# Performance work log

Measured on AMD Instinct MI355X. Metric: run time of the kernel, lower is better.

The kernel has to match this reference:

```python
import jax, jax.numpy as jnp
import numpy as np

B, S, D, H, HD, L, E, K, M, V = 1, 2048, 1024, 16, 64, 2, 8, 2, 768, 32000
EPS = 1e-06
THETA = 1000000.0


def rmsnorm(x, w, eps=EPS):
    xf = x.astype(jnp.float32)
    var = jnp.mean(xf * xf, axis=-1, keepdims=True)
    return (w * (xf * jax.lax.rsqrt(var + eps))).astype(x.dtype)


def apply_rope(x, cos, sin):
    # x: [B,S,H,HD], cos/sin: [S,HD]; rotate_half convention (HF Qwen3)
    c = cos[None, :, None, :]
    s = sin[None, :, None, :]
    x1, x2 = jnp.split(x, 2, axis=-1)
    rot = jnp.concatenate([-x2, x1], axis=-1)
    return x * c + rot * s


def setup_inputs() -> dict:
    key = jax.random.key(0)
    ks = jax.random.split(key, 16)
    std = 0.02
    inp = {}
    inp['input_ids'] = jax.random.randint(ks[0], (B, S), 0, V)
    inp['embed'] = jax.random.normal(ks[1], (V, D), jnp.float32) * std
    inp['wq'] = jax.random.normal(ks[2], (L, D, H * HD), jnp.float32) * std
    inp['wk'] = jax.random.normal(ks[3], (L, D, H * HD), jnp.float32) * std
    inp['wv'] = jax.random.normal(ks[4], (L, D, H * HD), jnp.float32) * std
    inp['wo'] = jax.random.normal(ks[5], (L, H * HD, D), jnp.float32) * std
    inp['q_norm_w'] = jnp.ones((L, HD), jnp.float32)
    inp['k_norm_w'] = jnp.ones((L, HD), jnp.float32)
    inp['attn_norm_w'] = jnp.ones((L, D), jnp.float32)
    inp['ffn_norm_w'] = jnp.ones((L, D), jnp.float32)
    inp['gate_w'] = jax.random.normal(ks[6], (L, D, E), jnp.float32) * std
    inp['w_gate'] = jax.random.normal(ks[7], (L, E, D, M), jnp.float32) * std
    inp['w_up'] = jax.random.normal(ks[8], (L, E, D, M), jnp.float32) * std
    inp['w_down'] = jax.random.normal(ks[9], (L, E, M, D), jnp.float32) * std
    inp['final_norm_w'] = jnp.ones((D,), jnp.float32)
    inp['out_w'] = jax.random.normal(ks[10], (D, V), jnp.float32) * (D ** -0.5)
    # rope cache: cos/sin with duplicated freqs (HF default rope)
    inv_freq = 1.0 / (THETA ** (jnp.arange(0, HD, 2, dtype=jnp.float32) / HD))
    freqs = jnp.outer(jnp.arange(S, dtype=jnp.float32), inv_freq)  # [S,HD/2]
    emb = jnp.concatenate([freqs, freqs], axis=-1)  # [S,HD]
    inp['cos'] = jnp.cos(emb)
    inp['sin'] = jnp.sin(emb)
    return inp


def reference(input_ids, embed, wq, wk, wv, wo, q_norm_w, k_norm_w, attn_norm_w,
              ffn_norm_w, gate_w, w_gate, w_up, w_down, final_norm_w, out_w, cos, sin):
    h = embed[input_ids]  # [B,S,D]
    causal = jnp.tril(jnp.ones((S, S), bool))[None, None]  # [1,1,S,S]
    scale = 1.0 / np.sqrt(HD)

    def layer(h, p):
        Wq, Wk, Wv, Wo, qn, kn, an, fn, gw, Wg, Wu, Wd = p
        # --- attention ---
        x = rmsnorm(h, an)
        q = (x @ Wq).reshape(B, S, H, HD)
        k = (x @ Wk).reshape(B, S, H, HD)
        v = (x @ Wv).reshape(B, S, H, HD)
        q = apply_rope(rmsnorm(q, qn), cos, sin)
        k = apply_rope(rmsnorm(k, kn), cos, sin)
        scores = jnp.einsum('bqhd,bkhd->bhqk', q, k) * scale
        scores = jnp.where(causal, scores, jnp.finfo(scores.dtype).min)
        attn = jax.nn.softmax(scores, axis=-1)
        o = jnp.einsum('bhqk,bkhd->bqhd', attn, v).reshape(B, S, H * HD) @ Wo
        h = h + o
        # --- sparse MoE ---
        x = rmsnorm(h, fn).reshape(-1, D)  # [T,D]
        probs = jax.nn.softmax((x @ gw).astype(jnp.float32), axis=-1)  # [T,E]
        vals, idx = jax.lax.top_k(probs, K)
        vals = vals / jnp.sum(vals, axis=-1, keepdims=True)  # norm_topk_prob=True
        T = x.shape[0]
        dense = jnp.zeros((T, E), x.dtype).at[jnp.arange(T)[:, None], idx].set(vals.astype(x.dtype))
        g = jnp.einsum('td,edm->tem', x, Wg)
        u = jnp.einsum('td,edm->tem', x, Wu)
        y = jnp.einsum('tem,emd->ted', jax.nn.silu(g) * u, Wd)
        moe = jnp.einsum('te,ted->td', dense, y).reshape(B, S, D)
        return h + moe, None

    h, _ = jax.lax.scan(layer, h, (wq, wk, wv, wo, q_norm_w, k_norm_w, attn_norm_w,
                                   ffn_norm_w, gate_w, w_gate, w_up, w_down))
    h = rmsnorm(h, final_norm_w)
    return h @ out_w  # [B,S,V]
```

## Files before the change

### kernel.cpp

```cpp
#include <hip/hip_runtime.h>
#include <hip/hip_bf16.h>


constexpr int S_ = 2048, D_ = 1024, H_ = 16, HD_ = 64, E_ = 8, MF_ = 768, V_ = 32000;

typedef short  short8 __attribute__((ext_vector_type(8)));
typedef float  f32x4  __attribute__((ext_vector_type(4)));

static __device__ __forceinline__ unsigned short f2bf(float f) {
    unsigned u = __float_as_uint(f);
    u += 0x7FFF + ((u >> 16) & 1);
    return (unsigned short)(u >> 16);
}

static __device__ __forceinline__ short8 u2s8(uint4 u) {
    union { uint4 a; short8 b; } x; x.a = u; return x.b;
}

__global__ __launch_bounds__(256) void k_gather(const int* __restrict__ ids,
                                                const float* __restrict__ emb,
                                                float* __restrict__ h) {
    int tok = blockIdx.x;
    int id  = ids[tok];
    const float4* src = (const float4*)(emb + (long)id * D_);
    float4*       dst = (float4*)(h + (long)tok * D_);
    dst[threadIdx.x] = src[threadIdx.x];
}

template <int BF>
__global__ __launch_bounds__(256) void k_rmsnorm(const float* __restrict__ in,
                                                 const float* __restrict__ w,
                                                 float* __restrict__ outf,
                                                 unsigned short* __restrict__ outb) {
    int row = blockIdx.x, t = threadIdx.x;
    float4 x = ((const float4*)(in + (long)row * D_))[t];
    float ss = x.x * x.x + x.y * x.y + x.z * x.z + x.w * x.w;
#pragma unroll
    for (int m = 32; m >= 1; m >>= 1) ss += __shfl_xor(ss, m);
    __shared__ float ps[4];
    if ((t & 63) == 0) ps[t >> 6] = ss;
    __syncthreads();
    float tot   = ps[0] + ps[1] + ps[2] + ps[3];
    float scale = 1.0f / sqrtf(tot * (1.0f / D_) + 1e-6f);
    float4 wv = ((const float4*)w)[t];
    float4 o;
    o.x = x.x * scale * wv.x; o.y = x.y * scale * wv.y;
    o.z = x.z * scale * wv.z; o.w = x.w * scale * wv.w;
    if (BF) {
        ushort4 ub;
        ub.x = f2bf(o.x); ub.y = f2bf(o.y); ub.z = f2bf(o.z); ub.w = f2bf(o.w);
        *(ushort4*)(outb + (long)row * D_ + t * 4) = ub;
    } else {
        ((float4*)(outf + (long)row * D_))[t] = o;
    }
}

__global__ __launch_bounds__(256) void k_qkrope(float* __restrict__ q, float* __restrict__ k,
                                                const float* __restrict__ qn,
                                                const float* __restrict__ kn,
                                                const float* __restrict__ cosb,
                                                const float* __restrict__ sinb) {
    int wid  = (blockIdx.x << 2) | (threadIdx.x >> 6);
    int lane = threadIdx.x & 63;
    int tensor = wid >> 15;
    int rem    = wid & 32767;
    int tok = rem >> 4, head = rem & 15;
    float* ptr = tensor ? k : q;
    const float* nw = tensor ? kn : qn;
    long off = ((long)tok * H_ + head) * HD_ + lane;
    float v = ptr[off];
    float ss = v * v;
#pragma unroll
    for (int m = 32; m >= 1; m >>= 1) ss += __shfl_xor(ss, m);
    float xn = v * (1.0f / sqrtf(ss * (1.0f / HD_) + 1e-6f)) * nw[lane];
    float other = __shfl_xor(xn, 32);
    float rot = (lane < 32) ? -other : other;
    ptr[off] = xn * cosb[tok * HD_ + lane] + rot * sinb[tok * HD_ + lane];
}

static __device__ __forceinline__ void splitpack2(float x0, float x1,
                                                  unsigned& wh, unsigned& wm,
                                                  unsigned& wl) {
    unsigned u0 = __float_as_uint(x0), u1 = __float_as_uint(x1);
    unsigned h0 = u0 & 0xFFFF0000u,    h1 = u1 & 0xFFFF0000u;
    float r0 = x0 - __uint_as_float(h0), r1 = x1 - __uint_as_float(h1);
    unsigned m0 = __float_as_uint(r0) & 0xFFFF0000u;
    unsigned m1 = __float_as_uint(r1) & 0xFFFF0000u;
    float s0 = r0 - __uint_as_float(m0), s1 = r1 - __uint_as_float(m1);
    unsigned l0 = __float_as_uint(s0),   l1 = __float_as_uint(s1);
    wh = (h0 >> 16) | h1;
    wm = (m0 >> 16) | m1;
    wl = (l0 >> 16) | (l1 & 0xFFFF0000u);
}

static __device__ __forceinline__ void split8(const float* v,
                                              uint4& qh, uint4& qm, uint4& ql) {
    unsigned ph[4], pm[4], pl[4];
#pragma unroll
    for (int j = 0; j < 4; j++) splitpack2(v[2 * j], v[2 * j + 1], ph[j], pm[j], pl[j]);
    qh = make_uint4(ph[0], ph[1], ph[2], ph[3]);
    qm = make_uint4(pm[0], pm[1], pm[2], pm[3]);
    ql = make_uint4(pl[0], pl[1], pl[2], pl[3]);
}

template <int IND, int EPI>
__global__ __launch_bounds__(256) void k_gemm_s6(const float* __restrict__ A,
                                                 const float* __restrict__ B0,
                                                 const float* __restrict__ B1,
                                                 const float* __restrict__ B2,
                                                 float* __restrict__ C,
                                                 const int* __restrict__ offs,
                                                 const int* __restrict__ rows,
                                                 const float* __restrict__ rwgt,
                                                 float* __restrict__ hout,
                                                 int Mtot, int N, int K,
                                                 long bStrideZ, long cStrideZ) {
    int z = blockIdx.z;
    int ms, me;
    if (offs) { ms = offs[z]; me = offs[z + 1]; }
    else      { ms = 0; me = Mtot; }
    int p0 = ms + blockIdx.y * 128;
    if (p0 >= me) return;
    const float* Bz;
    if (B1) Bz = (z == 0) ? B0 : (z == 1) ? B1 : B2;
    else    Bz = B0 + (long)z * bStrideZ;
    float* Cz = C ? (C + (long)z * cStrideZ) : nullptr;
    int n0 = blockIdx.x * 128;

    __shared__ __align__(16) unsigned short As[3][128][40];
    __shared__ __align__(16) unsigned short Bs[3][128][40];

    int t = threadIdx.x;
    int lane = t & 63, wave = t >> 6;
    int wm = (wave >> 1) * 64, wn = (wave & 1) * 64;
    int ln = lane & 15, lq = lane >> 4;

    f32x4 acc[4][4];
    f32x4 zero4 = {0.f, 0.f, 0.f, 0.f};
#pragma unroll
    for (int r = 0; r < 4; r++)
#pragma unroll
        for (int c = 0; c < 4; c++) acc[r][c] = zero4;

    int arow = t >> 1, ak0 = (t & 1) * 16;
    const float* aptr = nullptr;
    {
        int pA = p0 + arow;
        if (pA < me) {
            int srow = IND ? rows[pA] : pA;
            aptr = A + (long)srow * K + ak0;
        }
    }
    int brow = t >> 1, bk0 = (t & 1) * 16;
    const float* bbase = Bz + (n0 + brow);

    for (int k0 = 0; k0 < K; k0 += 32) {
        float va[16];
        if (aptr) {
#pragma unroll
            for (int c4 = 0; c4 < 4; c4++) {
                float4 f = *(const float4*)(aptr + k0 + c4 * 4);
                va[c4 * 4 + 0] = f.x; va[c4 * 4 + 1] = f.y;
                va[c4 * 4 + 2] = f.z; va[c4 * 4 + 3] = f.w;
            }
        } else {
#pragma unroll
            for (int j = 0; j < 16; j++) va[j] = 0.f;
        }
        uint4 ah0, am0, al0, ah1, am1, al1;
        split8(va,     ah0, am0, al0);
        split8(va + 8, ah1, am1, al1);
        float vb[16];
        {
            const float* bp = bbase + (long)(k0 + bk0) * N;
#pragma unroll
            for (int j = 0; j < 16; j++) vb[j] = bp[(long)j * N];
        }
        uint4 bh0, bm0, bl0, bh1, bm1, bl1;
        split8(vb,     bh0, bm0, bl0);
        split8(vb + 8, bh1, bm1, bl1);

        __syncthreads();
        *(uint4*)&As[0][arow][ak0]     = ah0;
        *(uint4*)&As[0][arow][ak0 + 8] = ah1;
        *(uint4*)&As[1][arow][ak0]     = am0;
        *(uint4*)&As[1][arow][ak0 + 8] = am1;
        *(uint4*)&As[2][arow][ak0]     = al0;
        *(uint4*)&As[2][arow][ak0 + 8] = al1;
        *(uint4*)&Bs[0][brow][bk0]     = bh0;
        *(uint4*)&Bs[0][brow][bk0 + 8] = bh1;
        *(uint4*)&Bs[1][brow][bk0]     = bm0;
        *(uint4*)&Bs[1][brow][bk0 + 8] = bm1;
        *(uint4*)&Bs[2][brow][bk0]     = bl0;
        *(uint4*)&Bs[2][brow][bk0 + 8] = bl1;
        __syncthreads();

        short8 fah[4], fam[4], fal[4];
#pragma unroll
        for (int r = 0; r < 4; r++) {
            fah[r] = *(const short8*)&As[0][wm + 16 * r + ln][lq * 8];
            fam[r] = *(const short8*)&As[1][wm + 16 * r + ln][lq * 8];
            fal[r] = *(const short8*)&As[2][wm + 16 * r + ln][lq * 8];
        }
#pragma unroll
        for (int c = 0; c < 4; c++) {
            short8 fbh = *(const short8*)&Bs[0][wn + 16 * c + ln][lq * 8];
            short8 fbm = *(const short8*)&Bs[1][wn + 16 * c + ln][lq * 8];
            short8 fbl = *(const short8*)&Bs[2][wn + 16 * c + ln][lq * 8];
#pragma unroll
            for (int r = 0; r < 4; r++) {
                f32x4 a2 = acc[r][c];
                a2 = __builtin_amdgcn_mfma_f32_16x16x32_bf16(fah[r], fbh, a2, 0, 0, 0);
                a2 = __builtin_amdgcn_mfma_f32_16x16x32_bf16(fah[r], fbm, a2, 0, 0, 0);
                a2 = __builtin_amdgcn_mfma_f32_16x16x32_bf16(fam[r], fbh, a2, 0, 0, 0);
                a2 = __builtin_amdgcn_mfma_f32_16x16x32_bf16(fah[r], fbl, a2, 0, 0, 0);
                a2 = __builtin_amdgcn_mfma_f32_16x16x32_bf16(fam[r], fbm, a2, 0, 0, 0);
                a2 = __builtin_amdgcn_mfma_f32_16x16x32_bf16(fal[r], fbh, a2, 0, 0, 0);
                acc[r][c] = a2;
            }
        }
    }

#pragma unroll
    for (int r = 0; r < 4; r++)
#pragma unroll
        for (int c = 0; c < 4; c++) {
            int rowb = wm + 16 * r + lq * 4;
            int col  = n0 + wn + 16 * c + ln;
#pragma unroll
            for (int i = 0; i < 4; i++) {
                int p = p0 + rowb + i;
                if (p >= me) continue;
                if (EPI == 2) {
                    atomicAdd(hout + (long)rows[p] * N + col, rwgt[p] * acc[r][c][i]);
                } else if (EPI == 1) {
                    float* cp = Cz + (long)p * N + col;
                    *cp += acc[r][c][i];
                } else {
                    Cz[(long)p * N + col] = acc[r][c][i];
                }
            }
        }
}

__global__ __launch_bounds__(256) void k_attn_mfma(const float* __restrict__ q,
                                                   const float* __restrict__ k,
                                                   const float* __restrict__ v,
                                                   float* __restrict__ o) {
    int head = blockIdx.y;
    int qi = ((blockIdx.y >> 3) & 1) ? (int)(gridDim.x - 1 - blockIdx.x) : (int)blockIdx.x;
    int q0 = qi * 64;

    __shared__ __align__(16) unsigned short Ks[3][64][72];
    __shared__ __align__(16) unsigned short Vt[3][64][72];
    __shared__ __align__(16) float Ps[64][68];

    int t = threadIdx.x;
    int lane = t & 63, w = t >> 6;
    int ln = lane & 15, lq = lane >> 4;

    short8 qh[2], qm[2], qlr[2];
    {
        const float* qp = q + ((long)(q0 + 16 * w + ln) * H_ + head) * HD_;
#pragma unroll
        for (int ks = 0; ks < 2; ks++) {
            float vq[8];
            float4 f0 = *(const float4*)(qp + 32 * ks + lq * 8);
            float4 f1 = *(const float4*)(qp + 32 * ks + lq * 8 + 4);
            vq[0] = f0.x; vq[1] = f0.y; vq[2] = f0.z; vq[3] = f0.w;
            vq[4] = f1.x; vq[5] = f1.y; vq[6] = f1.z; vq[7] = f1.w;
            uint4 hh, mm, ll;
            split8(vq, hh, mm, ll);
            qh[ks] = u2s8(hh); qm[ks] = u2s8(mm); qlr[ks] = u2s8(ll);
        }
    }

    f32x4 oc[4];
    f32x4 zero4 = {0.f, 0.f, 0.f, 0.f};
#pragma unroll
    for (int c = 0; c < 4; c++) oc[c] = zero4;
    float m_run[4], l_run[4];
#pragma unroll
    for (int i = 0; i < 4; i++) { m_run[i] = -3.402823466e38f; l_run[i] = 0.f; }

    for (int kt = 0; kt <= qi; kt++) {
        __syncthreads();
        {
            int kr = t >> 2, kq4 = (t & 3) * 16;
            const float* kp = k + ((long)(kt * 64 + kr) * H_ + head) * HD_ + kq4;
            float vk[16];
#pragma unroll
            for (int j = 0; j < 4; j++) {
                float4 f = *(const float4*)(kp + 4 * j);
                vk[4 * j + 0] = f.x; vk[4 * j + 1] = f.y;
                vk[4 * j + 2] = f.z; vk[4 * j + 3] = f.w;
            }
            uint4 h0, m0, l0, h1, m1, l1;
            split8(vk,     h0, m0, l0);
            split8(vk + 8, h1, m1, l1);
            *(uint4*)&Ks[0][kr][kq4]     = h0; *(uint4*)&Ks[0][kr][kq4 + 8] = h1;
            *(uint4*)&Ks[1][kr][kq4]     = m0; *(uint4*)&Ks[1][kr][kq4 + 8] = m1;
            *(uint4*)&Ks[2][kr][kq4]     = l0; *(uint4*)&Ks[2][kr][kq4 + 8] = l1;
            const float* vp = v + ((long)(kt * 64 + lane) * H_ + head) * HD_ + w * 16;
            float vvv[16];
#pragma unroll
            for (int j = 0; j < 4; j++) {
                float4 f = *(const float4*)(vp + 4 * j);
                vvv[4 * j + 0] = f.x; vvv[4 * j + 1] = f.y;
                vvv[4 * j + 2] = f.z; vvv[4 * j + 3] = f.w;
            }
#pragma unroll
            for (int j = 0; j < 16; j++) {
                float x = vvv[j];
                unsigned uu = __float_as_uint(x);
                unsigned hh = uu & 0xFFFF0000u;
                float rr = x - __uint_as_float(hh);
                unsigned mm2 = __float_as_uint(rr) & 0xFFFF0000u;
                float ss2 = rr - __uint_as_float(mm2);
                Vt[0][w * 16 + j][lane] = (unsigned short)(hh >> 16);
                Vt[1][w * 16 + j][lane] = (unsigned short)(mm2 >> 16);
                Vt[2][w * 16 + j][lane] = (unsigned short)(__float_as_uint(ss2) >> 16);
            }
        }
        __syncthreads();

        f32x4 sc[4];
#pragma unroll
        for (int c = 0; c < 4; c++) sc[c] = zero4;
#pragma unroll
        for (int ks = 0; ks < 2; ks++) {
#pragma unroll
            for (int c = 0; c < 4; c++) {
                const int co = 16 * c + ln, ko = 32 * ks + lq * 8;
                short8 bh = *(const short8*)&Ks[0][co][ko];
                short8 bm = *(const short8*)&Ks[1][co][ko];
                short8 bl = *(const short8*)&Ks[2][co][ko];
                f32x4 a2 = sc[c];
                a2 = __builtin_amdgcn_mfma_f32_16x16x32_bf16(qh[ks],  bh, a2, 0, 0, 0);
                a2 = __builtin_amdgcn_mfma_f32_16x16x32_bf16(qh[ks],  bm, a2, 0, 0, 0);
                a2 = __builtin_amdgcn_mfma_f32_16x16x32_bf16(qm[ks],  bh, a2, 0, 0, 0);
                a2 = __builtin_amdgcn_mfma_f32_16x16x32_bf16(qh[ks],  bl, a2, 0, 0, 0);
                a2 = __builtin_amdgcn_mfma_f32_16x16x32_bf16(qm[ks],  bm, a2, 0, 0, 0);
                a2 = __builtin_amdgcn_mfma_f32_16x16x32_bf16(qlr[ks], bh, a2, 0, 0, 0);
                sc[c] = a2;
            }
        }

#pragma unroll
        for (int i = 0; i < 4; i++) {
            int qg = q0 + 16 * w + 4 * lq + i;
            float mx = -3.402823466e38f;
#pragma unroll
            for (int c = 0; c < 4; c++) {
                int kvg = kt * 64 + 16 * c + ln;
                float s = sc[c][i] * 0.125f;
                s = (kvg <= qg) ? s : -3.402823466e38f;
                sc[c][i] = s;
                mx = fmaxf(mx, s);
            }
            mx = fmaxf(mx, __shfl_xor(mx, 1));
            mx = fmaxf(mx, __shfl_xor(mx, 2));
            mx = fmaxf(mx, __shfl_xor(mx, 4));
            mx = fmaxf(mx, __shfl_xor(mx, 8));
            float mn = fmaxf(m_run[i], mx);
            float al = expf(m_run[i] - mn);
            m_run[i] = mn;
            float sum = 0.f;
#pragma unroll
            for (int c = 0; c < 4; c++) {
                float e = expf(sc[c][i] - mn);
                Ps[16 * w + 4 * lq + i][16 * c + ln] = e;
                sum += e;
            }
            sum += __shfl_xor(sum, 1);
            sum += __shfl_xor(sum, 2);
            sum += __shfl_xor(sum, 4);
            sum += __shfl_xor(sum, 8);
            l_run[i] = l_run[i] * al + sum;
#pragma unroll
            for (int c = 0; c < 4; c++) oc[c][i] *= al;
        }

#pragma unroll
        for (int ks = 0; ks < 2; ks++) {
            float pv8[8];
            *(float4*)&pv8[0] = *(const float4*)&Ps[16 * w + ln][32 * ks + lq * 8];
            *(float4*)&pv8[4] = *(const float4*)&Ps[16 * w + ln][32 * ks + lq * 8 + 4];
            uint4 ph4, pm4, pl4;
            split8(pv8, ph4, pm4, pl4);
            short8 pah = u2s8(ph4), pam = u2s8(pm4), pal = u2s8(pl4);
#pragma unroll
            for (int c = 0; c < 4; c++) {
                const int co = 16 * c + ln, ko = 32 * ks + lq * 8;
                short8 bh = *(const short8*)&Vt[0][co][ko];
                short8 bm = *(const short8*)&Vt[1][co][ko];
                short8 bl = *(const short8*)&Vt[2][co][ko];
                f32x4 a2 = oc[c];
                a2 = __builtin_amdgcn_mfma_f32_16x16x32_bf16(pah, bh, a2, 0, 0, 0);
                a2 = __builtin_amdgcn_mfma_f32_16x16x32_bf16(pah, bm, a2, 0, 0, 0);
                a2 = __builtin_amdgcn_mfma_f32_16x16x32_bf16(pam, bh, a2, 0, 0, 0);
                a2 = __builtin_amdgcn_mfma_f32_16x16x32_bf16(pah, bl, a2, 0, 0, 0);
                a2 = __builtin_amdgcn_mfma_f32_16x16x32_bf16(pam, bm, a2, 0, 0, 0);
                a2 = __builtin_amdgcn_mfma_f32_16x16x32_bf16(pal, bh, a2, 0, 0, 0);
                oc[c] = a2;
            }
        }
    }

#pragma unroll
    for (int i = 0; i < 4; i++) {
        float invl = 1.0f / l_run[i];
        int qg = q0 + 16 * w + 4 * lq + i;
        float* op = o + ((long)qg * H_ + head) * HD_;
#pragma unroll
        for (int c = 0; c < 4; c++) op[16 * c + ln] = oc[c][i] * invl;
    }
}

__global__ __launch_bounds__(256) void k_router(const float* __restrict__ x,
                                                const float* __restrict__ gw,
                                                int* __restrict__ idx, float* __restrict__ wgt,
                                                int* __restrict__ cnt) {
    int tok  = (blockIdx.x << 2) | (threadIdx.x >> 6);
    int lane = threadIdx.x & 63;
    float acc[8] = {0.f, 0.f, 0.f, 0.f, 0.f, 0.f, 0.f, 0.f};
    for (int i = 0; i < 16; i++) {
        int d = lane + i * 64;
        float xv = x[(long)tok * D_ + d];
        const float* gp = gw + (long)d * E_;
#pragma unroll
        for (int e = 0; e < 8; e++) acc[e] = fmaf(xv, gp[e], acc[e]);
    }
#pragma unroll
    for (int e = 0; e < 8; e++)
#pragma unroll
        for (int m = 32; m >= 1; m >>= 1) acc[e] += __shfl_xor(acc[e], m);
    if (lane == 0) {
        int i1 = 0; float m1 = acc[0];
        for (int e = 1; e < 8; e++) if (acc[e] > m1) { m1 = acc[e]; i1 = e; }
        int i2 = -1; float m2 = -3.402823466e38f;
        for (int e = 0; e < 8; e++) if (e != i1 && acc[e] > m2) { m2 = acc[e]; i2 = e; }
        float w1 = 1.0f / (1.0f + expf(m2 - m1));
        idx[tok * 2] = i1; idx[tok * 2 + 1] = i2;
        wgt[tok * 2] = w1; wgt[tok * 2 + 1] = 1.0f - w1;
        atomicAdd(&cnt[i1], 1);
        atomicAdd(&cnt[i2], 1);
    }
}

__global__ void k_offsets(const int* __restrict__ cnt, int* __restrict__ off) {
    if (threadIdx.x == 0) {
        int run = 0;
        for (int e = 0; e < 8; e++) { off[e] = run; run += cnt[e]; }
        off[8] = run;
    }
}

__global__ __launch_bounds__(256) void k_scatter(const int* __restrict__ idx,
                                                 const float* __restrict__ wgt,
                                                 const int* __restrict__ off,
                                                 int* __restrict__ fill,
                                                 int* __restrict__ rows,
                                                 float* __restrict__ rwgt) {
    int tok = blockIdx.x * 256 + threadIdx.x;
#pragma unroll
    for (int j = 0; j < 2; j++) {
        int e = idx[tok * 2 + j];
        int pos = off[e] + atomicAdd(&fill[e], 1);
        rows[pos] = tok;
        rwgt[pos] = wgt[tok * 2 + j];
    }
}

__global__ __launch_bounds__(256) void k_silumul(const float* __restrict__ g,
                                                 const float* __restrict__ u,
                                                 float* __restrict__ z) {
    long i = (long)(blockIdx.x * 256 + threadIdx.x) * 4;
    float4 gv = *(const float4*)(g + i);
    float4 uv = *(const float4*)(u + i);
    float4 zv;
    zv.x = gv.x / (1.f + expf(-gv.x)) * uv.x;
    zv.y = gv.y / (1.f + expf(-gv.y)) * uv.y;
    zv.z = gv.z / (1.f + expf(-gv.z)) * uv.z;
    zv.w = gv.w / (1.f + expf(-gv.w)) * uv.w;
    *(float4*)(z + i) = zv;
}

__global__ __launch_bounds__(256) void k_transcast(const float* __restrict__ in,
                                                   unsigned short* __restrict__ out) {
    int c0 = blockIdx.x * 32;
    int r0 = blockIdx.y * 32;
    __shared__ __align__(16) float T[32][36];
    int t = threadIdx.x;
    {
        int row = t >> 3, cq = (t & 7) * 4;
        *(float4*)&T[row][cq] = *(const float4*)(in + (long)(r0 + row) * V_ + c0 + cq);
    }
    __syncthreads();
    {
        int n = t >> 3, kq = (t & 7) * 4;
        ushort4 u;
        u.x = f2bf(T[kq + 0][n]); u.y = f2bf(T[kq + 1][n]);
        u.z = f2bf(T[kq + 2][n]); u.w = f2bf(T[kq + 3][n]);
        *(ushort4*)(out + (long)(c0 + n) * D_ + r0 + kq) = u;
    }
}

__global__ __launch_bounds__(256) void k_gemm_bf16(const unsigned short* __restrict__ A,
                                                   const unsigned short* __restrict__ BT,
                                                   float* __restrict__ C) {
    int m0 = blockIdx.x * 128, n0 = blockIdx.y * 128;
    __shared__ __align__(16) unsigned short As[128][40];
    __shared__ __align__(16) unsigned short Bs[128][40];
    int t = threadIdx.x;
    int lane = t & 63, wave = t >> 6;
    int wm = (wave >> 1) * 64, wn = (wave & 1) * 64;
    int ln = lane & 15, lq = lane >> 4;
    f32x4 acc[4][4];
    f32x4 zero4 = {0.f, 0.f, 0.f, 0.f};
#pragma unroll
    for (int r = 0; r < 4; r++)
#pragma unroll
        for (int c = 0; c < 4; c++) acc[r][c] = zero4;
    int rowA = t >> 1;
    int q1 = (t * 2) & 3, q2 = (t * 2 + 1) & 3;
    for (int k0 = 0; k0 < 1024; k0 += 32) {
        const uint4* ap = (const uint4*)(A + (long)(m0 + rowA) * 1024 + k0);
        const uint4* bp = (const uint4*)(BT + (long)(n0 + rowA) * 1024 + k0);
        uint4 a0 = ap[q1], a1 = ap[q2];
        uint4 b0 = bp[q1], b1 = bp[q2];
        __syncthreads();
        *(uint4*)&As[rowA][q1 * 8] = a0;
        *(uint4*)&As[rowA][q2 * 8] = a1;
        *(uint4*)&Bs[rowA][q1 * 8] = b0;
        *(uint4*)&Bs[rowA][q2 * 8] = b1;
        __syncthreads();
        short8 a[4], b[4];
#pragma unroll
        for (int r = 0; r < 4; r++) a[r] = *(const short8*)&As[wm + 16 * r + ln][lq * 8];
#pragma unroll
        for (int c = 0; c < 4; c++) b[c] = *(const short8*)&Bs[wn + 16 * c + ln][lq * 8];
#pragma unroll
        for (int r = 0; r < 4; r++)
#pragma unroll
            for (int c = 0; c < 4; c++)
                acc[r][c] = __builtin_amdgcn_mfma_f32_16x16x32_bf16(a[r], b[c], acc[r][c], 0, 0, 0);
    }
#pragma unroll
    for (int r = 0; r < 4; r++)
#pragma unroll
        for (int c = 0; c < 4; c++) {
            int row = m0 + wm + 16 * r + lq * 4;
            int col = n0 + wn + 16 * c + ln;
#pragma unroll
            for (int i = 0; i < 4; i++)
                C[(long)(row + i) * V_ + col] = acc[r][c][i];
        }
}

extern "C" void kernel_launch(void* const* d_in, const int* in_sizes, int n_in,
                              void* d_out, int out_size, void* d_ws, size_t ws_size,
                              hipStream_t stream) {
    (void)in_sizes; (void)n_in; (void)out_size; (void)ws_size;
    const int*   ids   = (const int*)d_in[0];
    const float* embed = (const float*)d_in[1];
    const float* wq    = (const float*)d_in[2];
    const float* wk    = (const float*)d_in[3];
    const float* wv    = (const float*)d_in[4];
    const float* wo    = (const float*)d_in[5];
    const float* qnw   = (const float*)d_in[6];
    const float* knw   = (const float*)d_in[7];
    const float* anw   = (const float*)d_in[8];
    const float* fnw   = (const float*)d_in[9];
    const float* gatew = (const float*)d_in[10];
    const float* wgate = (const float*)d_in[11];
    const float* wup   = (const float*)d_in[12];
    const float* wdown = (const float*)d_in[13];
    const float* finw  = (const float*)d_in[14];
    const float* outw  = (const float*)d_in[15];
    const float* cosb  = (const float*)d_in[16];
    const float* sinb  = (const float*)d_in[17];
    float* out = (float*)d_out;

    char* w = (char*)d_ws;
    float* h  = (float*)(w);
    float* x  = (float*)(w + 8388608);
    float* q  = (float*)(w + 16777216);
    float* kk = (float*)(w + 25165824);
    float* vv = (float*)(w + 33554432);
    float* ao = (float*)(w + 41943040);
    float* g  = (float*)(w + 50331648);
    float* u  = (float*)(w + 62914560);
    float* z  = (float*)(w + 75497472);
    unsigned short* hn  = (unsigned short*)(w + 88080384);
    unsigned short* owT = (unsigned short*)(w + 16777216);
    char* rbase = w + 92274688;
    int*   idx  = (int*)(rbase);
    float* wgt  = (float*)(rbase + 16384);
    int*   cnt  = (int*)(rbase + 32768);
    int*   fill = (int*)(rbase + 32768 + 32);
    int*   offs = (int*)(rbase + 32768 + 64);
    int*   rows = (int*)(rbase + 32768 + 128);
    float* rwgt = (float*)(rbase + 32768 + 128 + 16384);

    k_gather<<<2048, 256, 0, stream>>>(ids, embed, h);

    for (int l = 0; l < 2; l++) {
        const float* wq_l = wq + (long)l * D_ * D_;
        const float* wk_l = wk + (long)l * D_ * D_;
        const float* wv_l = wv + (long)l * D_ * D_;
        const float* wo_l = wo + (long)l * D_ * D_;
        const float* an_l = anw + l * D_;
        const float* fn_l = fnw + l * D_;
        const float* qn_l = qnw + l * HD_;
        const float* kn_l = knw + l * HD_;
        const float* gw_l = gatew + (long)l * D_ * E_;
        const float* wg_l = wgate + (long)l * E_ * D_ * MF_;
        const float* wu_l = wup   + (long)l * E_ * D_ * MF_;
        const float* wd_l = wdown + (long)l * E_ * MF_ * D_;

        k_rmsnorm<0><<<2048, 256, 0, stream>>>(h, an_l, x, nullptr);
        k_gemm_s6<0, 0><<<dim3(8, 16, 3), 256, 0, stream>>>(x, wq_l, wk_l, wv_l, q,
            nullptr, nullptr, nullptr, nullptr, 2048, 1024, 1024, 0, 2048L * 1024);
        k_qkrope<<<16384, 256, 0, stream>>>(q, kk, qn_l, kn_l, cosb, sinb);
        k_attn_mfma<<<dim3(32, 16), 256, 0, stream>>>(q, kk, vv, ao);
        k_gemm_s6<0, 1><<<dim3(8, 16, 1), 256, 0, stream>>>(ao, wo_l, nullptr, nullptr, h,
            nullptr, nullptr, nullptr, nullptr, 2048, 1024, 1024, 0, 0);
        k_rmsnorm<0><<<2048, 256, 0, stream>>>(h, fn_l, x, nullptr);
        hipMemsetAsync(cnt, 0, 64, stream);
        k_router<<<512, 256, 0, stream>>>(x, gw_l, idx, wgt, cnt);
        k_offsets<<<1, 64, 0, stream>>>(cnt, offs);
        k_scatter<<<8, 256, 0, stream>>>(idx, wgt, offs, fill, rows, rwgt);
        k_gemm_s6<1, 0><<<dim3(6, 16, 8), 256, 0, stream>>>(x, wg_l, nullptr, nullptr, g,
            offs, rows, nullptr, nullptr, 4096, 768, 1024, (long)D_ * MF_, 0);
        k_gemm_s6<1, 0><<<dim3(6, 16, 8), 256, 0, stream>>>(x, wu_l, nullptr, nullptr, u,
            offs, rows, nullptr, nullptr, 4096, 768, 1024, (long)D_ * MF_, 0);
        k_silumul<<<3072, 256, 0, stream>>>(g, u, z);
        k_gemm_s6<0, 2><<<dim3(8, 16, 8), 256, 0, stream>>>(z, wd_l, nullptr, nullptr, nullptr,
            offs, rows, rwgt, h, 4096, 1024, 768, (long)MF_ * D_, 0);
    }

    k_rmsnorm<1><<<2048, 256, 0, stream>>>(h, finw, nullptr, hn);
    k_transcast<<<dim3(1000, 32), 256, 0, stream>>>(outw, owT);
    k_gemm_bf16<<<dim3(16, 250), 256, 0, stream>>>(hn, owT, out);
}
```

Before: 2.131 ms.

## Load GEMM A fragments directly from global and double-buffer B tiles

The split-bf16 grouped GEMM now loads A rows straight from global memory into MFMA fragments and splits them in registers, which removes the A shared-memory tile. B tiles are double-buffered in LDS so the next tile loads while the current one computes, with one barrier per half-step. The bf16 logits GEMM drops LDS entirely and register-prefetches fragments from global, ping-ponging between two sets. The cost is redundant global loads across waves that share rows, since there is no LDS reuse, and higher register pressure.

```diff
diff --git a/kernel.cpp b/kernel.cpp
--- a/kernel.cpp
+++ b/kernel.cpp
@@ -127,8 +127,7 @@
     float* Cz = C ? (C + (long)z * cStrideZ) : nullptr;
     int n0 = blockIdx.x * 128;
 
-    __shared__ __align__(16) unsigned short As[3][128][40];
-    __shared__ __align__(16) unsigned short Bs[3][128][40];
+    __shared__ __align__(16) unsigned short Bs[2][3][128][40];
 
     int t = threadIdx.x;
     int lane = t & 63, wave = t >> 6;
@@ -142,71 +141,56 @@
 #pragma unroll
         for (int c = 0; c < 4; c++) acc[r][c] = zero4;
 
-    int arow = t >> 1, ak0 = (t & 1) * 16;
-    const float* aptr = nullptr;
-    {
-        int pA = p0 + arow;
-        if (pA < me) {
-            int srow = IND ? rows[pA] : pA;
-            aptr = A + (long)srow * K + ak0;
+    const float* aptr[4];
+#pragma unroll
+    for (int r = 0; r < 4; r++) {
+        int p = p0 + wm + 16 * r + ln;
+        aptr[r] = nullptr;
+        if (p < me) {
+            int srow = IND ? rows[p] : p;
+            aptr[r] = A + (long)srow * K + lq * 8;
         }
     }
     int brow = t >> 1, bk0 = (t & 1) * 16;
     const float* bbase = Bz + (n0 + brow);
 
-    for (int k0 = 0; k0 < K; k0 += 32) {
-        float va[16];
-        if (aptr) {
-#pragma unroll
-            for (int c4 = 0; c4 < 4; c4++) {
-                float4 f = *(const float4*)(aptr + k0 + c4 * 4);
-                va[c4 * 4 + 0] = f.x; va[c4 * 4 + 1] = f.y;
-                va[c4 * 4 + 2] = f.z; va[c4 * 4 + 3] = f.w;
-            }
-        } else {
-#pragma unroll
-            for (int j = 0; j < 16; j++) va[j] = 0.f;
-        }
-        uint4 ah0, am0, al0, ah1, am1, al1;
-        split8(va,     ah0, am0, al0);
-        split8(va + 8, ah1, am1, al1);
+    auto bload = [&](int kk, uint4* bh, uint4* bm, uint4* bl) {
         float vb[16];
-        {
-            const float* bp = bbase + (long)(k0 + bk0) * N;
-#pragma unroll
-            for (int j = 0; j < 16; j++) vb[j] = bp[(long)j * N];
-        }
-        uint4 bh0, bm0, bl0, bh1, bm1, bl1;
-        split8(vb,     bh0, bm0, bl0);
-        split8(vb + 8, bh1, bm1, bl1);
-
-        __syncthreads();
-        *(uint4*)&As[0][arow][ak0]     = ah0;
-        *(uint4*)&As[0][arow][ak0 + 8] = ah1;
-        *(uint4*)&As[1][arow][ak0]     = am0;
-        *(uint4*)&As[1][arow][ak0 + 8] = am1;
-        *(uint4*)&As[2][arow][ak0]     = al0;
-        *(uint4*)&As[2][arow][ak0 + 8] = al1;
-        *(uint4*)&Bs[0][brow][bk0]     = bh0;
-        *(uint4*)&Bs[0][brow][bk0 + 8] = bh1;
-        *(uint4*)&Bs[1][brow][bk0]     = bm0;
-        *(uint4*)&Bs[1][brow][bk0 + 8] = bm1;
-        *(uint4*)&Bs[2][brow][bk0]     = bl0;
-        *(uint4*)&Bs[2][brow][bk0 + 8] = bl1;
-        __syncthreads();
-
-        short8 fah[4], fam[4], fal[4];
+        const float* bp = bbase + (long)(kk + bk0) * N;
+#pragma unroll
+        for (int j = 0; j < 16; j++) vb[j] = bp[(long)j * N];
+        split8(vb,     bh[0], bm[0], bl[0]);
+        split8(vb + 8, bh[1], bm[1], bl[1]);
+    };
+    auto bwrite = [&](int buf, const uint4* bh, const uint4* bm, const uint4* bl) {
+        *(uint4*)&Bs[buf][0][brow][bk0]     = bh[0];
+        *(uint4*)&Bs[buf][0][brow][bk0 + 8] = bh[1];
+        *(uint4*)&Bs[buf][1][brow][bk0]     = bm[0];
+        *(uint4*)&Bs[buf][1][brow][bk0 + 8] = bm[1];
+        *(uint4*)&Bs[buf][2][brow][bk0]     = bl[0];
+        *(uint4*)&Bs[buf][2][brow][bk0 + 8] = bl[1];
+    };
+    auto aload = [&](int kk, short8* fah, short8* fam, short8* fal) {
 #pragma unroll
         for (int r = 0; r < 4; r++) {
-            fah[r] = *(const short8*)&As[0][wm + 16 * r + ln][lq * 8];
-            fam[r] = *(const short8*)&As[1][wm + 16 * r + ln][lq * 8];
-            fal[r] = *(const short8*)&As[2][wm + 16 * r + ln][lq * 8];
-        }
+            float va[8] = {0.f, 0.f, 0.f, 0.f, 0.f, 0.f, 0.f, 0.f};
+            if (aptr[r]) {
+                float4 f0 = *(const float4*)(aptr[r] + kk);
+                float4 f1 = *(const float4*)(aptr[r] + kk + 4);
+                va[0] = f0.x; va[1] = f0.y; va[2] = f0.z; va[3] = f0.w;
+                va[4] = f1.x; va[5] = f1.y; va[6] = f1.z; va[7] = f1.w;
+            }
+            uint4 hh, mm, ll;
+            split8(va, hh, mm, ll);
+            fah[r] = u2s8(hh); fam[r] = u2s8(mm); fal[r] = u2s8(ll);
+        }
+    };
+    auto domfma = [&](int buf, const short8* fah, const short8* fam, const short8* fal) {
 #pragma unroll
         for (int c = 0; c < 4; c++) {
-            short8 fbh = *(const short8*)&Bs[0][wn + 16 * c + ln][lq * 8];
-            short8 fbm = *(const short8*)&Bs[1][wn + 16 * c + ln][lq * 8];
-            short8 fbl = *(const short8*)&Bs[2][wn + 16 * c + ln][lq * 8];
+            short8 fbh = *(const short8*)&Bs[buf][0][wn + 16 * c + ln][lq * 8];
+            short8 fbm = *(const short8*)&Bs[buf][1][wn + 16 * c + ln][lq * 8];
+            short8 fbl = *(const short8*)&Bs[buf][2][wn + 16 * c + ln][lq * 8];
 #pragma unroll
             for (int r = 0; r < 4; r++) {
                 f32x4 a2 = acc[r][c];
@@ -219,6 +203,30 @@
                 acc[r][c] = a2;
             }
         }
+    };
+
+    {
+        uint4 bh[2], bm[2], bl[2];
+        bload(0, bh, bm, bl);
+        bwrite(0, bh, bm, bl);
+    }
+    __syncthreads();
+
+    for (int k0 = 0; k0 < K; k0 += 64) {
+        short8 fah[4], fam[4], fal[4];
+        uint4 bh[2], bm[2], bl[2];
+        aload(k0, fah, fam, fal);
+        bload(k0 + 32, bh, bm, bl);
+        domfma(0, fah, fam, fal);
+        bwrite(1, bh, bm, bl);
+        __syncthreads();
+        aload(k0 + 32, fah, fam, fal);
+        int kn = k0 + 64;
+        bool more = kn < K;
+        if (more) bload(kn, bh, bm, bl);
+        domfma(1, fah, fam, fal);
+        if (more) bwrite(0, bh, bm, bl);
+        __syncthreads();
     }
 
 #pragma unroll
@@ -510,8 +518,6 @@
                                                    const unsigned short* __restrict__ BT,
                                                    float* __restrict__ C) {
     int m0 = blockIdx.x * 128, n0 = blockIdx.y * 128;
-    __shared__ __align__(16) unsigned short As[128][40];
-    __shared__ __align__(16) unsigned short Bs[128][40];
     int t = threadIdx.x;
     int lane = t & 63, wave = t >> 6;
     int wm = (wave >> 1) * 64, wn = (wave & 1) * 64;
@@ -522,30 +528,44 @@
     for (int r = 0; r < 4; r++)
 #pragma unroll
         for (int c = 0; c < 4; c++) acc[r][c] = zero4;
-    int rowA = t >> 1;
-    int q1 = (t * 2) & 3, q2 = (t * 2 + 1) & 3;
-    for (int k0 = 0; k0 < 1024; k0 += 32) {
-        const uint4* ap = (const uint4*)(A + (long)(m0 + rowA) * 1024 + k0);
-        const uint4* bp = (const uint4*)(BT + (long)(n0 + rowA) * 1024 + k0);
-        uint4 a0 = ap[q1], a1 = ap[q2];
-        uint4 b0 = bp[q1], b1 = bp[q2];
-        __syncthreads();
-        *(uint4*)&As[rowA][q1 * 8] = a0;
-        *(uint4*)&As[rowA][q2 * 8] = a1;
-        *(uint4*)&Bs[rowA][q1 * 8] = b0;
-        *(uint4*)&Bs[rowA][q2 * 8] = b1;
-        __syncthreads();
-        short8 a[4], b[4];
-#pragma unroll
-        for (int r = 0; r < 4; r++) a[r] = *(const short8*)&As[wm + 16 * r + ln][lq * 8];
-#pragma unroll
-        for (int c = 0; c < 4; c++) b[c] = *(const short8*)&Bs[wn + 16 * c + ln][lq * 8];
+
+    const unsigned short* ap[4];
+    const unsigned short* bp[4];
+#pragma unroll
+    for (int r = 0; r < 4; r++) ap[r] = A  + (long)(m0 + wm + 16 * r + ln) * 1024 + lq * 8;
+#pragma unroll
+    for (int c = 0; c < 4; c++) bp[c] = BT + (long)(n0 + wn + 16 * c + ln) * 1024 + lq * 8;
+
+    short8 a0[4], b0[4], a1[4], b1[4];
+#pragma unroll
+    for (int r = 0; r < 4; r++) a0[r] = *(const short8*)(ap[r]);
+#pragma unroll
+    for (int c = 0; c < 4; c++) b0[c] = *(const short8*)(bp[c]);
+
+#pragma unroll 1
+    for (int k0 = 0; k0 < 1024; k0 += 64) {
+        int k1 = k0 + 32;
+#pragma unroll
+        for (int r = 0; r < 4; r++) a1[r] = *(const short8*)(ap[r] + k1);
+#pragma unroll
+        for (int c = 0; c < 4; c++) b1[c] = *(const short8*)(bp[c] + k1);
 #pragma unroll
         for (int r = 0; r < 4; r++)
 #pragma unroll
             for (int c = 0; c < 4; c++)
-                acc[r][c] = __builtin_amdgcn_mfma_f32_16x16x32_bf16(a[r], b[c], acc[r][c], 0, 0, 0);
-    }
+                acc[r][c] = __builtin_amdgcn_mfma_f32_16x16x32_bf16(a0[r], b0[c], acc[r][c], 0, 0, 0);
+        int k2 = (k0 + 64) & 1023;
+#pragma unroll
+        for (int r = 0; r < 4; r++) a0[r] = *(const short8*)(ap[r] + k2);
+#pragma unroll
+        for (int c = 0; c < 4; c++) b0[c] = *(const short8*)(bp[c] + k2);
+#pragma unroll
+        for (int r = 0; r < 4; r++)
+#pragma unroll
+            for (int c = 0; c < 4; c++)
+                acc[r][c] = __builtin_amdgcn_mfma_f32_16x16x32_bf16(a1[r], b1[c], acc[r][c], 0, 0, 0);
+    }
+
 #pragma unroll
     for (int r = 0; r < 4; r++)
 #pragma unroll
```

Result: slower. 3.336 ms (+56.6%).

## Pre-split and transpose weights into bf16 planes before each GEMM

Applied to the files above, without the earlier changes.

Adds a k_wsplit kernel that transposes each fp32 weight matrix and splits it into hi/mid/lo bf16 planes laid out N-major. The GEMM then loads B tiles with contiguous 16-byte vector loads instead of strided scalar fp32 loads followed by per-block splitting. This removes redundant splitting across M-tiles and uncoalesced B reads. The cost is extra launches and a full read and write of the weights every call, and plane buffers are aliased into workspace regions, which risks overlap.

```diff
diff --git a/kernel.cpp b/kernel.cpp
--- a/kernel.cpp
+++ b/kernel.cpp
@@ -103,27 +103,54 @@
     ql = make_uint4(pl[0], pl[1], pl[2], pl[3]);
 }
 
+__global__ __launch_bounds__(256) void k_wsplit(const float* __restrict__ in,
+                                                unsigned short* __restrict__ out,
+                                                int N, int K,
+                                                long inStrideZ, long outStrideZ) {
+    int z = blockIdx.z;
+    const float* inz = in + (long)z * inStrideZ;
+    unsigned short* outz = out + (long)z * outStrideZ;
+    int n0 = blockIdx.x * 32, k0 = blockIdx.y * 32;
+    __shared__ float T[32][33];
+    int t = threadIdx.x;
+    {
+        int row = t >> 3, c4 = (t & 7) * 4;
+        *(float4*)&T[row][c4] = *(const float4*)(inz + (long)(k0 + row) * N + n0 + c4);
+    }
+    __syncthreads();
+    int n = t >> 3, kq = (t & 7) * 4;
+    float v0 = T[kq][n], v1 = T[kq + 1][n], v2 = T[kq + 2][n], v3 = T[kq + 3][n];
+    unsigned h01, m01, l01, h23, m23, l23;
+    splitpack2(v0, v1, h01, m01, l01);
+    splitpack2(v2, v3, h23, m23, l23);
+    long base = (long)(n0 + n) * K + k0 + kq;
+    long pk = (long)N * K;
+    *(uint2*)(outz + base)          = make_uint2(h01, h23);
+    *(uint2*)(outz + pk + base)     = make_uint2(m01, m23);
+    *(uint2*)(outz + 2 * pk + base) = make_uint2(l01, l23);
+}
+
 template <int IND, int EPI>
 __global__ __launch_bounds__(256) void k_gemm_s6(const float* __restrict__ A,
-                                                 const float* __restrict__ B0,
-                                                 const float* __restrict__ B1,
-                                                 const float* __restrict__ B2,
+                                                 const unsigned short* __restrict__ BplA,
+                                                 const unsigned short* __restrict__ BplB,
+                                                 int zsplit,
                                                  float* __restrict__ C,
                                                  const int* __restrict__ offs,
                                                  const int* __restrict__ rows,
                                                  const float* __restrict__ rwgt,
                                                  float* __restrict__ hout,
                                                  int Mtot, int N, int K,
-                                                 long bStrideZ, long cStrideZ) {
+                                                 long cStrideZ) {
     int z = blockIdx.z;
     int ms, me;
     if (offs) { ms = offs[z]; me = offs[z + 1]; }
     else      { ms = 0; me = Mtot; }
     int p0 = ms + blockIdx.y * 128;
     if (p0 >= me) return;
-    const float* Bz;
-    if (B1) Bz = (z == 0) ? B0 : (z == 1) ? B1 : B2;
-    else    Bz = B0 + (long)z * bStrideZ;
+    long planeSz = (long)N * K;
+    const unsigned short* bpl = (z < zsplit) ? BplA + (long)z * 3 * planeSz
+                                             : BplB + (long)(z - zsplit) * 3 * planeSz;
     float* Cz = C ? (C + (long)z * cStrideZ) : nullptr;
     int n0 = blockIdx.x * 128;
 
@@ -142,17 +169,28 @@
 #pragma unroll
         for (int c = 0; c < 4; c++) acc[r][c] = zero4;
 
-    int arow = t >> 1, ak0 = (t & 1) * 16;
+    int arow = t >> 1, ak0 = (t & 1) * 8;
+    arow = t >> 1; int akf = (t & 1) * 16;
     const float* aptr = nullptr;
     {
         int pA = p0 + arow;
         if (pA < me) {
             int srow = IND ? rows[pA] : pA;
-            aptr = A + (long)srow * K + ak0;
-        }
-    }
-    int brow = t >> 1, bk0 = (t & 1) * 16;
-    const float* bbase = Bz + (n0 + brow);
+            aptr = A + (long)srow * K + akf;
+        }
+    }
+    (void)ak0;
+
+    const unsigned short* bsrc[6];
+    unsigned short* bdst[6];
+#pragma unroll
+    for (int j = 0; j < 6; j++) {
+        int id = t + 256 * j;
+        int plane = id >> 9, rem = id & 511;
+        int brow = rem >> 2, bq = rem & 3;
+        bsrc[j] = bpl + (long)plane * planeSz + (long)(n0 + brow) * K + bq * 8;
+        bdst[j] = &Bs[plane][brow][bq * 8];
+    }
 
     for (int k0 = 0; k0 < K; k0 += 32) {
         float va[16];
@@ -170,29 +208,19 @@
         uint4 ah0, am0, al0, ah1, am1, al1;
         split8(va,     ah0, am0, al0);
         split8(va + 8, ah1, am1, al1);
-        float vb[16];
-        {
-            const float* bp = bbase + (long)(k0 + bk0) * N;
-#pragma unroll
-            for (int j = 0; j < 16; j++) vb[j] = bp[(long)j * N];
-        }
-        uint4 bh0, bm0, bl0, bh1, bm1, bl1;
-        split8(vb,     bh0, bm0, bl0);
-        split8(vb + 8, bh1, bm1, bl1);
+        uint4 bv[6];
+#pragma unroll
+        for (int j = 0; j < 6; j++) bv[j] = *(const uint4*)(bsrc[j] + k0);
 
         __syncthreads();
-        *(uint4*)&As[0][arow][ak0]     = ah0;
-        *(uint4*)&As[0][arow][ak0 + 8] = ah1;
-        *(uint4*)&As[1][arow][ak0]     = am0;
-        *(uint4*)&As[1][arow][ak0 + 8] = am1;
-        *(uint4*)&As[2][arow][ak0]     = al0;
-        *(uint4*)&As[2][arow][ak0 + 8] = al1;
-        *(uint4*)&Bs[0][brow][bk0]     = bh0;
-        *(uint4*)&Bs[0][brow][bk0 + 8] = bh1;
-        *(uint4*)&Bs[1][brow][bk0]     = bm0;
-        *(uint4*)&Bs[1][brow][bk0 + 8] = bm1;
-        *(uint4*)&Bs[2][brow][bk0]     = bl0;
-        *(uint4*)&Bs[2][brow][bk0 + 8] = bl1;
+        *(uint4*)&As[0][arow][akf]     = ah0;
+        *(uint4*)&As[0][arow][akf + 8] = ah1;
+        *(uint4*)&As[1][arow][akf]     = am0;
+        *(uint4*)&As[1][arow][akf + 8] = am1;
+        *(uint4*)&As[2][arow][akf]     = al0;
+        *(uint4*)&As[2][arow][akf + 8] = al1;
+#pragma unroll
+        for (int j = 0; j < 6; j++) *(uint4*)bdst[j] = bv[j];
         __syncthreads();
 
         short8 fah[4], fam[4], fal[4];
@@ -603,41 +631,70 @@
     int*   rows = (int*)(rbase + 32768 + 128);
     float* rwgt = (float*)(rbase + 32768 + 128 + 16384);
 
+    unsigned short* qkvpl = (unsigned short*)(w + 50331648);
+    unsigned short* wopl  = (unsigned short*)(w + 50331648);
+    unsigned short* mplA  = (unsigned short*)(w + 16777216);
+    unsigned short* wgplB = (unsigned short*)(w + 62914560);
+    unsigned short* wuplB = (unsigned short*)(w + 75497472);
+    unsigned short* wdplB = (unsigned short*)(w + 50331648);
+
+    const long DxD = (long)D_ * D_;
+    const long DxM = (long)D_ * MF_;
+    const long EPL_DM = 3L * MF_ * D_;
+
     k_gather<<<2048, 256, 0, stream>>>(ids, embed, h);
 
     for (int l = 0; l < 2; l++) {
-        const float* wq_l = wq + (long)l * D_ * D_;
-        const float* wk_l = wk + (long)l * D_ * D_;
-        const float* wv_l = wv + (long)l * D_ * D_;
-        const float* wo_l = wo + (long)l * D_ * D_;
+        const float* wq_l = wq + (long)l * DxD;
+        const float* wk_l = wk + (long)l * DxD;
+        const float* wv_l = wv + (long)l * DxD;
+        const float* wo_l = wo + (long)l * DxD;
         const float* an_l = anw + l * D_;
         const float* fn_l = fnw + l * D_;
         const float* qn_l = qnw + l * HD_;
         const float* kn_l = knw + l * HD_;
         const float* gw_l = gatew + (long)l * D_ * E_;
-        const float* wg_l = wgate + (long)l * E_ * D_ * MF_;
-        const float* wu_l = wup   + (long)l * E_ * D_ * MF_;
-        const float* wd_l = wdown + (long)l * E_ * MF_ * D_;
+        const float* wg_l = wgate + (long)l * E_ * DxM;
+        const float* wu_l = wup   + (long)l * E_ * DxM;
+        const float* wd_l = wdown + (long)l * E_ * DxM;
 
         k_rmsnorm<0><<<2048, 256, 0, stream>>>(h, an_l, x, nullptr);
-        k_gemm_s6<0, 0><<<dim3(8, 16, 3), 256, 0, stream>>>(x, wq_l, wk_l, wv_l, q,
-            nullptr, nullptr, nullptr, nullptr, 2048, 1024, 1024, 0, 2048L * 1024);
+
+        k_wsplit<<<dim3(32, 32, 1), 256, 0, stream>>>(wq_l, qkvpl,             1024, 1024, 0, 0);
+        k_wsplit<<<dim3(32, 32, 1), 256, 0, stream>>>(wk_l, qkvpl + 3 * DxD,   1024, 1024, 0, 0);
+        k_wsplit<<<dim3(32, 32, 1), 256, 0, stream>>>(wv_l, qkvpl + 6 * DxD,   1024, 1024, 0, 0);
+        k_gemm_s6<0, 0><<<dim3(8, 16, 3), 256, 0, stream>>>(x, qkvpl, qkvpl, 8, q,
+            nullptr, nullptr, nullptr, nullptr, 2048, 1024, 1024, 2048L * 1024);
+
+        k_wsplit<<<dim3(32, 32, 1), 256, 0, stream>>>(wo_l, wopl, 1024, 1024, 0, 0);
+
         k_qkrope<<<16384, 256, 0, stream>>>(q, kk, qn_l, kn_l, cosb, sinb);
         k_attn_mfma<<<dim3(32, 16), 256, 0, stream>>>(q, kk, vv, ao);
-        k_gemm_s6<0, 1><<<dim3(8, 16, 1), 256, 0, stream>>>(ao, wo_l, nullptr, nullptr, h,
-            nullptr, nullptr, nullptr, nullptr, 2048, 1024, 1024, 0, 0);
+        k_gemm_s6<0, 1><<<dim3(8, 16, 1), 256, 0, stream>>>(ao, wopl, wopl, 8, h,
+            nullptr, nullptr, nullptr, nullptr, 2048, 1024, 1024, 0);
+
         k_rmsnorm<0><<<2048, 256, 0, stream>>>(h, fn_l, x, nullptr);
         hipMemsetAsync(cnt, 0, 64, stream);
         k_router<<<512, 256, 0, stream>>>(x, gw_l, idx, wgt, cnt);
         k_offsets<<<1, 64, 0, stream>>>(cnt, offs);
         k_scatter<<<8, 256, 0, stream>>>(idx, wgt, offs, fill, rows, rwgt);
-        k_gemm_s6<1, 0><<<dim3(6, 16, 8), 256, 0, stream>>>(x, wg_l, nullptr, nullptr, g,
-            offs, rows, nullptr, nullptr, 4096, 768, 1024, (long)D_ * MF_, 0);
-        k_gemm_s6<1, 0><<<dim3(6, 16, 8), 256, 0, stream>>>(x, wu_l, nullptr, nullptr, u,
-            offs, rows, nullptr, nullptr, 4096, 768, 1024, (long)D_ * MF_, 0);
+
+        k_wsplit<<<dim3(24, 32, 6), 256, 0, stream>>>(wg_l,             mplA,  768, 1024, DxM, EPL_DM);
+        k_wsplit<<<dim3(24, 32, 2), 256, 0, stream>>>(wg_l + 6 * DxM,   wgplB, 768, 1024, DxM, EPL_DM);
+        k_gemm_s6<1, 0><<<dim3(6, 16, 8), 256, 0, stream>>>(x, mplA, wgplB, 6, g,
+            offs, rows, nullptr, nullptr, 4096, 768, 1024, 0);
+
+        k_wsplit<<<dim3(24, 32, 6), 256, 0, stream>>>(wu_l,             mplA,  768, 1024, DxM, EPL_DM);
+        k_wsplit<<<dim3(24, 32, 2), 256, 0, stream>>>(wu_l + 6 * DxM,   wuplB, 768, 1024, DxM, EPL_DM);
+        k_gemm_s6<1, 0><<<dim3(6, 16, 8), 256, 0, stream>>>(x, mplA, wuplB, 6, u,
+            offs, rows, nullptr, nullptr, 4096, 768, 1024, 0);
+
         k_silumul<<<3072, 256, 0, stream>>>(g, u, z);
-        k_gemm_s6<0, 2><<<dim3(8, 16, 8), 256, 0, stream>>>(z, wd_l, nullptr, nullptr, nullptr,
-            offs, rows, rwgt, h, 4096, 1024, 768, (long)MF_ * D_, 0);
+
+        k_wsplit<<<dim3(32, 24, 6), 256, 0, stream>>>(wd_l,             mplA,  1024, 768, DxM, EPL_DM);
+        k_wsplit<<<dim3(32, 24, 2), 256, 0, stream>>>(wd_l + 6 * DxM,   wdplB, 1024, 768, DxM, EPL_DM);
+        k_gemm_s6<0, 2><<<dim3(8, 16, 8), 256, 0, stream>>>(z, mplA, wdplB, 6, nullptr,
+            offs, rows, rwgt, h, 4096, 1024, 768, 0);
     }
 
     k_rmsnorm<1><<<2048, 256, 0, stream>>>(h, finw, nullptr, hn);
```

Measured after the change: 2.724 ms. 1.28x slower.
